# Kernel tuning notes

Measured on AMD Instinct MI355X. Metric: run time of the kernel, lower is better.

## Reference

```python
import jax, jax.numpy as jnp
import numpy as np

NT = ['SB', 'PQ', 'PV', 'NB']
SIZES = {'SB': 4000, 'PQ': 30000, 'PV': 15000, 'NB': 12000}
ETYPES = [('PV','SB'),('SB','PQ'),('SB','NB'),('PV','PQ'),('NB','PQ'),('PQ','NB'),('SB','PV'),('PQ','SB'),('NB','SB'),('PQ','PV'),('PV','NB'),('NB','PV'),('PV','PV'),('PQ','PQ'),('NB','NB')]
L, H, O, F, E, ED = 2, 128, 64, 8, 150000, 2
T = len(ETYPES)


def setup_inputs():
    key = jax.random.key(0)
    ks = iter(jax.random.split(key, 80))
    inp = {}
    for nt in NT:
        inp['x_' + nt] = jax.random.normal(next(ks), (SIZES[nt], 4), jnp.float32)
        inp['c_' + nt] = jax.random.normal(next(ks), (SIZES[nt], 4), jnp.float32)
    ei = []
    for (s, d) in ETYPES:
        ei.append(jnp.stack([jax.random.randint(next(ks), (E,), 0, SIZES[s]),
                             jax.random.randint(next(ks), (E,), 0, SIZES[d])]))
    inp['edge_index'] = jnp.stack(ei).astype(jnp.int32)  # [T, 2, E]
    inp['edge_attr'] = jax.random.normal(next(ks), (T, E, ED), jnp.float32)
    p = lambda k, *s: jax.random.normal(k, s, jnp.float32) * 0.1
    inp['Wq'] = p(next(ks), L, T, F, H); inp['bq'] = jnp.zeros((L, T, H), jnp.float32)
    inp['Wk'] = p(next(ks), L, T, F, H); inp['bk'] = jnp.zeros((L, T, H), jnp.float32)
    inp['Wv'] = p(next(ks), L, T, F, H); inp['bv'] = jnp.zeros((L, T, H), jnp.float32)
    inp['We'] = p(next(ks), L, T, ED, H); inp['be'] = jnp.zeros((L, T, H), jnp.float32)
    inp['Ws'] = p(next(ks), L, T, F, H); inp['bs'] = jnp.zeros((L, T, H), jnp.float32)
    inp['W_lin'] = p(next(ks), 2, O); inp['b_lin'] = jnp.zeros((O,), jnp.float32)
    inp['W_fc'] = p(next(ks), len(NT), O, O); inp['b_fc'] = jnp.zeros((len(NT), O), jnp.float32)
    inp['W_lin2'] = p(next(ks), 2, O); inp['b_lin2'] = jnp.zeros((O,), jnp.float32)
    return inp


def _tconv(xs, xd, src, dst, ea, Wq, bq, Wk, bk, Wv, bv, We, be, Ws, bs):
    # PyG TransformerConv, heads=1, edge_dim=2, root_weight=True, beta=False
    nd = xd.shape[0]
    q = xd @ Wq + bq            # [Nd, H]
    k = xs @ Wk + bk            # [Ns, H]
    v = xs @ Wv + bv            # [Ns, H]
    e = ea @ We + be            # [E, H]
    kj = k[src] + e
    vj = v[src] + e
    logit = (q[dst] * kj).sum(-1) / np.float32(np.sqrt(q.shape[-1]))  # [E]
    m = jax.ops.segment_max(logit, dst, num_segments=nd)
    pe = jnp.exp(logit - m[dst])
    den = jax.ops.segment_sum(pe, dst, num_segments=nd)
    alpha = pe / (den[dst] + 1e-16)  # PyG softmax epsilon
    agg = jax.ops.segment_sum(alpha[:, None] * vj, dst, num_segments=nd)
    return agg + xd @ Ws + bs   # skip connection (lin_skip)


def _group_sum(xs):
    # 'group': cat on node axis, split channels in half (P/Q), sum each half
    out = jnp.concatenate(xs, axis=0)
    half = out.shape[1] // 2
    return jnp.stack([out[:, :half].sum(1), out[:, half:].sum(1)], axis=1)  # [M, 2]


def reference(x_SB, x_PQ, x_PV, x_NB, c_SB, c_PQ, c_PV, c_NB, edge_index, edge_attr,
              Wq, bq, Wk, bk, Wv, bv, We, be, Ws, bs,
              W_lin, b_lin, W_fc, b_fc, W_lin2, b_lin2):
    xmap = {'SB': (x_SB, c_SB), 'PQ': (x_PQ, c_PQ), 'PV': (x_PV, c_PV), 'NB': (x_NB, c_NB)}
    x = {nt: jnp.concatenate(xmap[nt], axis=1) for nt in NT}  # [N, 8]
    outs = {nt: [] for nt in NT}
    for i in range(L):
        for t, (s, d) in enumerate(ETYPES):
            outs[d].append(_tconv(x[s], x[d], edge_index[t, 0], edge_index[t, 1], edge_attr[t],
                                  Wq[i, t], bq[i, t], Wk[i, t], bk[i, t], Wv[i, t], bv[i, t],
                                  We[i, t], be[i, t], Ws[i, t], bs[i, t]))
    agg = {nt: jax.nn.elu(_group_sum(outs[nt]) @ W_lin + b_lin) for nt in NT}
    # HeteroMinMaxNorm with running_min=0, running_max=1, momentum=0.1 (updated then used)
    xc = jnp.concatenate([agg[nt] for nt in NT], axis=0)
    rmin = 0.1 * xc.min()
    rmax = 0.9 + 0.1 * xc.max()
    xsc = (xc - rmin) / (rmax - rmin + 1e-5) * 2.0 - 1.0
    sizes = [agg[nt].shape[0] for nt in NT]
    splits = jnp.split(xsc, np.cumsum(sizes)[:-1].tolist(), axis=0)
    nrm = dict(zip(NT, splits))
    node_lists = {nt: [] for nt in NT}
    for i in range(L):
        for j, nt in enumerate(NT):
            node_lists[nt].append(jax.nn.elu(nrm[nt] @ W_fc[j] + b_fc[j]))
    final = [jax.nn.elu(_group_sum(node_lists[nt]) @ W_lin2 + b_lin2) for nt in NT]
    return jnp.concatenate(final, axis=0)  # [960000, 64]
```

## Files before the change

### kernel.cpp

```cpp
#include <hip/hip_runtime.h>
#include <hip/hip_fp16.h>
#include <math.h>

#define NE 150000

__constant__ int c_stype[15] = {2,0,0,2,3,1,0,1,3,1,2,3,2,1,3};
__constant__ int c_dtype[15] = {0,1,3,1,1,3,2,0,0,2,3,2,2,1,3};
__constant__ int c_slot[15]  = {0,0,0,1,2,1,0,1,2,1,2,2,3,3,3};
__constant__ int c_N[4]      = {4000,30000,15000,12000};
__constant__ int c_xoff[4]   = {0,4000,34000,49000};
__constant__ int c_cnt[4]    = {3,4,4,4};
__constant__ int c_aggoff[4] = {0,24000,264000,384000};
__constant__ int c_outoff[4] = {0,48000,528000,768000};
__constant__ int c_aggrows[4]= {24000,240000,120000,96000};
__constant__ int c_lT[4] = {7,10,9,9};
__constant__ int c_tprefix[16] = {0,32,62,86,116,146,170,200,232,264,294,318,348,378,408,432};
__constant__ int c_toff2[15] = {0,4001,34002,46003,76004,106005,118006,133007,137008,141009,156010,168011,183012,198013,228014};

typedef _Float16 f16x8 __attribute__((ext_vector_type(8)));
typedef float f32x4 __attribute__((ext_vector_type(4)));

__device__ __forceinline__ float eluf(float x){ return x > 0.0f ? x : expm1f(x); }
__device__ __forceinline__ float elufast(float x){ return x > 0.0f ? x : __expf(x)-1.0f; }
__device__ __forceinline__ unsigned encf(float f){ unsigned u=__float_as_uint(f); return (u&0x80000000u)? ~u : (u|0x80000000u); }
__device__ __forceinline__ float decf(unsigned u){ return __uint_as_float((u&0x80000000u)? (u^0x80000000u) : ~u); }
__device__ __forceinline__ float RL(float v, int l){ return __uint_as_float(__builtin_amdgcn_readlane(__float_as_uint(v), l)); }

__device__ __forceinline__ float dot128(const float* __restrict__ a, const float* __restrict__ b){
  const float4* a4 = (const float4*)a; const float4* b4 = (const float4*)b;
  float s = 0.f;
  #pragma unroll
  for (int h=0; h<32; h++){
    float4 A=a4[h], B=b4[h];
    s = fmaf(A.x,B.x,s); s = fmaf(A.y,B.y,s); s = fmaf(A.z,B.z,s); s = fmaf(A.w,B.w,s);
  }
  return s;
}
__device__ __forceinline__ void halfsum(const float* __restrict__ a, float& s0, float& s1){
  const float4* a4 = (const float4*)a;
  float x0=0.f, x1=0.f;
  #pragma unroll
  for (int h=0; h<16; h++){ float4 A=a4[h]; x0 += A.x+A.y+A.z+A.w; }
  #pragma unroll
  for (int h=16; h<32; h++){ float4 A=a4[h]; x1 += A.x+A.y+A.z+A.w; }
  s0=x0; s1=x1;
}

#define CHUNK 18750

__global__ __launch_bounds__(1024) void k_front(
    const float* __restrict__ xSB, const float* __restrict__ cSB,
    const float* __restrict__ xPQ, const float* __restrict__ cPQ,
    const float* __restrict__ xPV, const float* __restrict__ cPV,
    const float* __restrict__ xNB, const float* __restrict__ cNB,
    const int* __restrict__ eidx,
    const float* __restrict__ Wq, const float* __restrict__ bq,
    const float* __restrict__ Wk, const float* __restrict__ bk,
    const float* __restrict__ Wv, const float* __restrict__ bv,
    const float* __restrict__ We, const float* __restrict__ be,
    const float* __restrict__ Ws, const float* __restrict__ bs,
    float* __restrict__ xall, float* __restrict__ par, int* __restrict__ gcnt8){
  const int b = blockIdx.x;
  if (b < 60){
    const int n = b*1024 + threadIdx.x;
    if (n >= 61000) return;
    const float *xp, *cp; int local;
    if (n < 4000)      { xp=xSB; cp=cSB; local=n; }
    else if (n < 34000){ xp=xPQ; cp=cPQ; local=n-4000; }
    else if (n < 49000){ xp=xPV; cp=cPV; local=n-34000; }
    else               { xp=xNB; cp=cNB; local=n-49000; }
    float4 a = ((const float4*)xp)[local];
    float4 bb = ((const float4*)cp)[local];
    ((float4*)xall)[n*2+0] = a;
    ((float4*)xall)[n*2+1] = bb;
  } else if (b < 90){
    const int c = b - 60, tid = threadIdx.x;
    if (tid >= 128) return;
    const float* wq = Wq + (size_t)c*1024;
    const float* wk = Wk + (size_t)c*1024;
    const float* wv = Wv + (size_t)c*1024;
    const float* ws = Ws + (size_t)c*1024;
    const float* we = We + (size_t)c*256;
    const float* vbq = bq + (size_t)c*128;
    const float* vbk = bk + (size_t)c*128;
    const float* vbv = bv + (size_t)c*128;
    const float* vbe = be + (size_t)c*128;
    const float* vbs = bs + (size_t)c*128;
    float* P = par + (size_t)c*160;
    if (tid < 64){
      int fd = tid>>3, fs = tid&7;
      P[tid] = dot128(wq + fd*128, wk + fs*128);
      return;
    }
    const int job = tid - 64, grp = job>>3, f = job&7;
    if (grp==0) P[64+f] = dot128(wq + f*128, vbk);
    else if (grp==1) P[72+f] = dot128(wk + f*128, vbq);
    else if (grp==2) P[80+f] = dot128(wq + f*128, we);
    else if (grp==3) P[88+f] = dot128(wq + f*128, we+128);
    else if (grp==4) P[96+f] = dot128(wq + f*128, vbe);
    else if (grp==5){ float s0,s1; halfsum(wv + f*128, s0,s1); P[104+f]=s0; P[112+f]=s1; }
    else if (grp==6){ float s0,s1; halfsum(ws + f*128, s0,s1); P[120+f]=s0; P[128+f]=s1; }
    else {
      if (f==0){ P[136] = dot128(vbq, vbk);
                 float a,bb; halfsum(vbs, a,bb); P[148]=a; P[149]=bb; }
      else if (f==1) P[137] = dot128(vbq, we);
      else if (f==2) P[138] = dot128(vbq, we+128);
      else if (f==3) P[139] = dot128(vbq, vbe);
      else if (f==4){ float a=0.f,bb=0.f; for(int h=0;h<64;h++){a+=we[h]; bb+=we[64+h];} P[140]=a; P[141]=bb; }
      else if (f==5){ float a=0.f,bb=0.f; for(int h=0;h<64;h++){a+=we[128+h]; bb+=we[192+h];} P[142]=a; P[143]=bb; }
      else if (f==6){ float a,bb; halfsum(vbv, a,bb); P[144]=a; P[145]=bb; }
      else          { float a,bb; halfsum(vbe, a,bb); P[146]=a; P[147]=bb; }
    }
  } else {
    const int cb = b - 90;
    const int t = cb / 8, chunk = cb % 8;
    const int lT = c_lT[c_dtype[t]];
    __shared__ int scnt[32];
    if (threadIdx.x < 32) scnt[threadIdx.x] = 0;
    __syncthreads();
    const int* __restrict__ dstp = eidx + (size_t)(t*2+1)*NE;
    const int e0 = chunk*CHUNK, e1 = min(NE, e0+CHUNK);
    for (int e=e0+threadIdx.x; e<e1; e+=1024) atomicAdd(&scnt[dstp[e]>>lT], 1);
    __syncthreads();
    if (threadIdx.x < 32) gcnt8[(t*8 + chunk)*32 + threadIdx.x] = scnt[threadIdx.x];
  }
}

__global__ void k_scan(const int* __restrict__ gcnt8, int* __restrict__ gcnt,
                       int* __restrict__ gofs, int* __restrict__ gcur,
                       unsigned* __restrict__ mm){
  const int t = threadIdx.x;
  if (t == 16){ mm[0] = 0xFFFFFFFFu; }
  else if (t == 17){ mm[1] = 0u; }
  if (t >= 15) return;
  const int b0 = c_tprefix[t], b1 = c_tprefix[t+1];
  int run = t*NE;
  for (int b=b0; b<b1; b++){
    const int tile = b - b0;
    int c0 = 0;
    #pragma unroll
    for (int c=0; c<8; c++) c0 += gcnt8[(t*8 + c)*32 + tile];
    gcnt[b] = c0;
    gofs[b] = run; gcur[b] = run;
    run += c0;
  }
}

__global__ __launch_bounds__(1024) void k_scatter(const int* __restrict__ eidx,
    const float* __restrict__ eattr,
    int* __restrict__ gcur, uint2* __restrict__ ebuf){
  const int t = blockIdx.y;
  const int lT = c_lT[c_dtype[t]];
  const int tmask = (1<<lT) - 1;
  __shared__ int lcnt[32], lbase[32];
  if (threadIdx.x < 32) lcnt[threadIdx.x] = 0;
  __syncthreads();
  const int* __restrict__ dstp = eidx + (size_t)(t*2+1)*NE;
  const int* __restrict__ srcp = eidx + (size_t)(t*2)*NE;
  const float2* __restrict__ ea2 = (const float2*)eattr + (size_t)t*NE;
  const int e0 = blockIdx.x*CHUNK, e1 = min(NE, e0+CHUNK);
  for (int e=e0+threadIdx.x; e<e1; e+=1024) atomicAdd(&lcnt[dstp[e]>>lT], 1);
  __syncthreads();
  if (threadIdx.x < 32){
    int cchk = lcnt[threadIdx.x];
    lbase[threadIdx.x] = cchk > 0 ? atomicAdd(&gcur[c_tprefix[t]+threadIdx.x], cchk) : 0;
  }
  __syncthreads();
  if (threadIdx.x < 32) lcnt[threadIdx.x] = 0;
  __syncthreads();
  for (int e=e0+threadIdx.x; e<e1; e+=1024){
    const int d = dstp[e];
    const int tile = d>>lT, dl = d & tmask;
    const int pos = lbase[tile] + atomicAdd(&lcnt[tile], 1);
    const float2 ea = ea2[e];
    __half2 h2 = __floats2half2_rn(ea.x, ea.y);
    ebuf[pos] = make_uint2(((unsigned)srcp[e]<<10) | (unsigned)dl, *(unsigned*)&h2);
  }
}

__global__ __launch_bounds__(1024) void k_tsort(
    const uint2* __restrict__ ebuf,
    const int* __restrict__ gofs, const int* __restrict__ gcnt,
    uint2* __restrict__ erec, int* __restrict__ gs2, int* __restrict__ glen){
  const int b = blockIdx.x;
  int t = 0;
  while (b >= c_tprefix[t+1]) ++t;
  const int tile = b - c_tprefix[t];
  const int dt = c_dtype[t];
  const int N = c_N[dt];
  const int lT = c_lT[dt];
  const int nbase = tile << lT;
  const int tileN = min(1<<lT, N - nbase);
  const int tid = threadIdx.x;
  const int lane = tid & 63, wid = tid >> 6;

  __shared__ int cnt[1024];
  __shared__ int wsum[16];

  cnt[tid] = 0;
  __syncthreads();
  const int start = gofs[b], count = gcnt[b];
  for (int k=tid; k<count; k+=1024) atomicAdd(&cnt[ebuf[start+k].x & 1023u], 1);
  __syncthreads();
  const int v = cnt[tid];
  int inc = v;
  #pragma unroll
  for (int off=1; off<64; off<<=1){ int u = __shfl_up(inc, off); if (lane>=off) inc += u; }
  if (lane==63) wsum[wid] = inc;
  __syncthreads();
  if (tid==0){ int r=0; for (int k=0;k<16;k++){ int x=wsum[k]; wsum[k]=r; r+=x; } }
  __syncthreads();
  const int pref = wsum[wid] + inc - v;
  if (tid < tileN){
    gs2 [c_toff2[t] + nbase + tid] = start + pref;
    glen[c_toff2[t] + nbase + tid] = v;
  }
  cnt[tid] = pref;
  __syncthreads();
  for (int k=tid; k<count; k+=1024){
    const uint2 u2 = ebuf[start+k];
    const int dl = u2.x & 1023u;
    const int pos = start + atomicAdd(&cnt[dl], 1);
    erec[pos] = make_uint2(u2.x >> 10, u2.y);
  }
}

__global__ __launch_bounds__(256) void k_gather(
    const int* __restrict__ gs2, const int* __restrict__ glen,
    const uint2* __restrict__ erec,
    const float* __restrict__ xall, const float* __restrict__ par,
    const float* __restrict__ Wl, const float* __restrict__ bl,
    float* __restrict__ g, unsigned* __restrict__ mm){
  const int t = blockIdx.y;
  const int dt = c_dtype[t], st = c_stype[t];
  const int N = c_N[dt];
  if (blockIdx.x*256 >= N) return;
  __shared__ float sA[160], sB[160];
  __shared__ float wlb[192];
  __shared__ float smin[4], smax[4];
  const int tid = threadIdx.x;
  if (tid < 160){ sA[tid] = par[(size_t)t*160 + tid]; sB[tid] = par[(size_t)(15+t)*160 + tid]; }
  if (tid < 192) wlb[tid] = (tid<128)? Wl[tid] : bl[tid-128];
  __syncthreads();
  const int n = blockIdx.x*256 + tid;
  const bool valid = n < N;
  float lmin = 3.4e38f, lmax = -3.4e38f;
  if (valid){
    const float4* xdp = (const float4*)(xall + (size_t)(c_xoff[dt]+n)*8);
    float4 b0v = xdp[0], b1v = xdp[1];
    float xd[8] = {b0v.x,b0v.y,b0v.z,b0v.w,b1v.x,b1v.y,b1v.z,b1v.w};
    float r2a[8], r2b[8];
    #pragma unroll
    for (int fs=0; fs<8; fs++){
      float a = sA[72+fs], bb = sB[72+fs];
      #pragma unroll
      for (int fd=0; fd<8; fd++){ a = fmaf(xd[fd], sA[fd*8+fs], a); bb = fmaf(xd[fd], sB[fd*8+fs], bb); }
      r2a[fs]=a; r2b[fs]=bb;
    }
    float t0a=sA[137], t1a=sA[138], tba=sA[139], u0a=sA[136];
    float t0b=sB[137], t1b=sB[138], tbb=sB[139], u0b=sB[136];
    #pragma unroll
    for (int f=0;f<8;f++){
      t0a = fmaf(xd[f], sA[80+f], t0a);  t0b = fmaf(xd[f], sB[80+f], t0b);
      t1a = fmaf(xd[f], sA[88+f], t1a);  t1b = fmaf(xd[f], sB[88+f], t1b);
      tba = fmaf(xd[f], sA[96+f], tba);  tbb = fmaf(xd[f], sB[96+f], tbb);
      u0a = fmaf(xd[f], sA[64+f], u0a);  u0b = fmaf(xd[f], sB[64+f], u0b);
    }
    const float accda = u0a + tba, accdb = u0b + tbb;
    const int o = c_toff2[t];
    const int js = gs2[o+n], je = js + glen[o+n];
    float denA=0.f, n0A=0.f, n1A=0.f;
    float denB=0.f, n0B=0.f, n1B=0.f;
    if (je > js){
      uint2 rec = erec[js];
      const float4* xp0 = (const float4*)(xall + (size_t)(c_xoff[st]+(int)rec.x)*8);
      float4 xa = xp0[0], xb = xp0[1];
      for (int j=js; j<je; j++){
        const int jn = (j+1 < je) ? j+1 : j;
        const uint2 recn = erec[jn];
        const float4* xpn = (const float4*)(xall + (size_t)(c_xoff[st]+(int)recn.x)*8);
        const float4 xan = xpn[0], xbn = xpn[1];
        const __half2 h2 = *(const __half2*)&rec.y;
        const float eax = __low2float(h2), eay = __high2float(h2);
        float xs[8] = {xa.x,xa.y,xa.z,xa.w,xb.x,xb.y,xb.z,xb.w};
        float accA = accda, accB = accdb;
        float v0A = fmaf(eax, sA[140], fmaf(eay, sA[142], sA[144]+sA[146]));
        float v1A = fmaf(eax, sA[141], fmaf(eay, sA[143], sA[145]+sA[147]));
        float v0B = fmaf(eax, sB[140], fmaf(eay, sB[142], sB[144]+sB[146]));
        float v1B = fmaf(eax, sB[141], fmaf(eay, sB[143], sB[145]+sB[147]));
        #pragma unroll
        for (int f=0;f<8;f++){
          accA = fmaf(xs[f], r2a[f], accA);   accB = fmaf(xs[f], r2b[f], accB);
          v0A  = fmaf(xs[f], sA[104+f], v0A); v0B  = fmaf(xs[f], sB[104+f], v0B);
          v1A  = fmaf(xs[f], sA[112+f], v1A); v1B  = fmaf(xs[f], sB[112+f], v1B);
        }
        accA = fmaf(eax, t0a, fmaf(eay, t1a, accA));
        accB = fmaf(eax, t0b, fmaf(eay, t1b, accB));
        const float peA = __expf(accA * 0.08838834764831845f);
        const float peB = __expf(accB * 0.08838834764831845f);
        denA += peA; n0A = fmaf(peA, v0A, n0A); n1A = fmaf(peA, v1A, n1A);
        denB += peB; n0B = fmaf(peB, v0B, n0B); n1B = fmaf(peB, v1B, n1B);
        rec = recn; xa = xan; xb = xbn;
      }
    }
    const float invA = 1.0f/(denA + 1e-16f);
    const float invB = 1.0f/(denB + 1e-16f);
    float s0a = fmaf(n0A, invA, sA[148]), s1a = fmaf(n1A, invA, sA[149]);
    float s0b = fmaf(n0B, invB, sB[148]), s1b = fmaf(n1B, invB, sB[149]);
    #pragma unroll
    for (int f=0;f<8;f++){
      s0a = fmaf(xd[f], sA[120+f], s0a); s1a = fmaf(xd[f], sA[128+f], s1a);
      s0b = fmaf(xd[f], sB[120+f], s0b); s1b = fmaf(xd[f], sB[128+f], s1b);
    }
    const int baseA = c_aggoff[dt] + (0*c_cnt[dt] + c_slot[t])*N + n;
    const int baseB = c_aggoff[dt] + (1*c_cnt[dt] + c_slot[t])*N + n;
    ((float2*)g)[baseA] = make_float2(s0a, s1a);
    ((float2*)g)[baseB] = make_float2(s0b, s1b);
    #pragma unroll
    for (int h=0;h<64;h++){
      float za = fmaf(s0a, wlb[h], fmaf(s1a, wlb[64+h], wlb[128+h]));
      float zb = fmaf(s0b, wlb[h], fmaf(s1b, wlb[64+h], wlb[128+h]));
      lmin = fminf(lmin, fminf(za,zb)); lmax = fmaxf(lmax, fmaxf(za,zb));
    }
  }
  #pragma unroll
  for (int m=32;m>=1;m>>=1){
    lmin = fminf(lmin, __shfl_xor(lmin,m));
    lmax = fmaxf(lmax, __shfl_xor(lmax,m));
  }
  const int wv = tid>>6;
  if ((tid&63)==0){ smin[wv]=lmin; smax[wv]=lmax; }
  __syncthreads();
  if (tid==0){
    float mn = fminf(fminf(smin[0],smin[1]), fminf(smin[2],smin[3]));
    float mx = fmaxf(fmaxf(smax[0],smax[1]), fmaxf(smax[2],smax[3]));
    atomicMin(&mm[0], encf(mn));
    atomicMax(&mm[1], encf(mx));
  }
}

__global__ __launch_bounds__(256) void k_final(
    const float* __restrict__ g, const unsigned* __restrict__ mm,
    const float* __restrict__ Wl, const float* __restrict__ bl,
    const float* __restrict__ Wfc, const float* __restrict__ bfc,
    const float* __restrict__ Wl2, const float* __restrict__ bl2,
    float* __restrict__ out){
  const int gw = blockIdx.x*4 + (threadIdx.x>>6);
  const int l  = threadIdx.x & 63;
  const int lr = l & 15, lg = l >> 4;
  int nt, wo;
  if (gw < 375)       { nt=0; wo=0; }
  else if (gw < 4125) { nt=1; wo=375; }
  else if (gw < 6000) { nt=2; wo=4125; }
  else                { nt=3; wo=6000; }
  const int R = c_aggrows[nt];
  const int r0 = (gw - wo)*64;
  const float zmin = decf(mm[0]), zmax = decf(mm[1]);
  const float rmin = 0.1f*eluf(zmin);
  const float rmax = 0.9f + 0.1f*eluf(zmax);
  const float s2 = 2.0f/(rmax - rmin + 1e-5f);
  const float cc = fmaf(-rmin, s2, -1.0f);
  float wl0v[2][8], wl1v[2][8], blv[2][8];
  #pragma unroll
  for (int kk=0; kk<2; kk++){
    const int hb = kk*32 + lg*8;
    const float4 a0 = *(const float4*)&Wl[hb],    a1 = *(const float4*)&Wl[hb+4];
    const float4 b0 = *(const float4*)&Wl[64+hb], b1 = *(const float4*)&Wl[64+hb+4];
    const float4 c0 = *(const float4*)&bl[hb],    c1 = *(const float4*)&bl[hb+4];
    wl0v[kk][0]=a0.x; wl0v[kk][1]=a0.y; wl0v[kk][2]=a0.z; wl0v[kk][3]=a0.w;
    wl0v[kk][4]=a1.x; wl0v[kk][5]=a1.y; wl0v[kk][6]=a1.z; wl0v[kk][7]=a1.w;
    wl1v[kk][0]=b0.x; wl1v[kk][1]=b0.y; wl1v[kk][2]=b0.z; wl1v[kk][3]=b0.w;
    wl1v[kk][4]=b1.x; wl1v[kk][5]=b1.y; wl1v[kk][6]=b1.z; wl1v[kk][7]=b1.w;
    blv[kk][0]=c0.x;  blv[kk][1]=c0.y;  blv[kk][2]=c0.z;  blv[kk][3]=c0.w;
    blv[kk][4]=c1.x;  blv[kk][5]=c1.y;  blv[kk][6]=c1.z;  blv[kk][7]=c1.w;
  }
  const float* __restrict__ W = Wfc + (size_t)nt*4096;
  f16x8 bfrag[2][4];
  #pragma unroll
  for (int kk=0; kk<2; kk++){
    #pragma unroll
    for (int ntl=0; ntl<4; ntl++){
      #pragma unroll
      for (int j=0; j<8; j++){
        const int h = kk*32 + lg*8 + j;
        bfrag[kk][ntl][j] = (_Float16)W[h*64 + ntl*16 + lr];
      }
    }
  }
  const float bf0 = bfc[nt*64 + lr],      bf1 = bfc[nt*64 + 16 + lr];
  const float bf2 = bfc[nt*64 + 32 + lr], bf3 = bfc[nt*64 + 48 + lr];
  const float2* __restrict__ g2p = (const float2*)g + c_aggoff[nt] + r0;
  const float wl20 = Wl2[l], wl21 = Wl2[64+l], bl2v = bl2[l];
  float* __restrict__ o1 = out + ((size_t)c_outoff[nt] + r0)*64 + l;
  float* __restrict__ o2 = o1 + (size_t)R*64;
  #pragma unroll
  for (int mt=0; mt<4; mt++){
    const float2 gv = g2p[mt*16 + lr];
    f16x8 af0, af1;
    #pragma unroll
    for (int j=0; j<8; j++){
      const float z0 = fmaf(gv.x, wl0v[0][j], fmaf(gv.y, wl1v[0][j], blv[0][j]));
      const float z1 = fmaf(gv.x, wl0v[1][j], fmaf(gv.y, wl1v[1][j], blv[1][j]));
      af0[j] = (_Float16)fmaf(elufast(z0), s2, cc);
      af1[j] = (_Float16)fmaf(elufast(z1), s2, cc);
    }
    f32x4 d0 = {0.f,0.f,0.f,0.f}, d1 = {0.f,0.f,0.f,0.f};
    f32x4 d2 = {0.f,0.f,0.f,0.f}, d3 = {0.f,0.f,0.f,0.f};
    d0 = __builtin_amdgcn_mfma_f32_16x16x32_f16(af0, bfrag[0][0], d0, 0,0,0);
    d1 = __builtin_amdgcn_mfma_f32_16x16x32_f16(af0, bfrag[0][1], d1, 0,0,0);
    d2 = __builtin_amdgcn_mfma_f32_16x16x32_f16(af0, bfrag[0][2], d2, 0,0,0);
    d3 = __builtin_amdgcn_mfma_f32_16x16x32_f16(af0, bfrag[0][3], d3, 0,0,0);
    d0 = __builtin_amdgcn_mfma_f32_16x16x32_f16(af1, bfrag[1][0], d0, 0,0,0);
    d1 = __builtin_amdgcn_mfma_f32_16x16x32_f16(af1, bfrag[1][1], d1, 0,0,0);
    d2 = __builtin_amdgcn_mfma_f32_16x16x32_f16(af1, bfrag[1][2], d2, 0,0,0);
    d3 = __builtin_amdgcn_mfma_f32_16x16x32_f16(af1, bfrag[1][3], d3, 0,0,0);
    float ph0[4], ph1[4];
    #pragma unroll
    for (int reg=0; reg<4; reg++){
      float p0 = elufast(d0[reg] + bf0) + elufast(d1[reg] + bf1);
      float p1 = elufast(d2[reg] + bf2) + elufast(d3[reg] + bf3);
      p0 += __shfl_xor(p0,1); p0 += __shfl_xor(p0,2); p0 += __shfl_xor(p0,4); p0 += __shfl_xor(p0,8);
      p1 += __shfl_xor(p1,1); p1 += __shfl_xor(p1,2); p1 += __shfl_xor(p1,4); p1 += __shfl_xor(p1,8);
      ph0[reg] = p0; ph1[reg] = p1;
    }
    #pragma unroll
    for (int rt=0; rt<16; rt++){
      const int r = mt*16 + rt;
      const float h0r = RL(ph0[rt&3], (rt>>2)<<4);
      const float h1r = RL(ph1[rt&3], (rt>>2)<<4);
      const float f = elufast(fmaf(h0r, wl20, fmaf(h1r, wl21, bl2v)));
      o1[(size_t)r*64] = f;
      o2[(size_t)r*64] = f;
    }
  }
}

extern "C" void kernel_launch(void* const* d_in, const int* in_sizes, int n_in,
                              void* d_out, int out_size, void* d_ws, size_t ws_size,
                              hipStream_t stream) {
  const float* xSB = (const float*)d_in[0];
  const float* cSB = (const float*)d_in[1];
  const float* xPQ = (const float*)d_in[2];
  const float* cPQ = (const float*)d_in[3];
  const float* xPV = (const float*)d_in[4];
  const float* cPV = (const float*)d_in[5];
  const float* xNB = (const float*)d_in[6];
  const float* cNB = (const float*)d_in[7];
  const int*   eidx = (const int*)d_in[8];
  const float* eattr= (const float*)d_in[9];
  const float* Wq = (const float*)d_in[10];
  const float* bq = (const float*)d_in[11];
  const float* Wk = (const float*)d_in[12];
  const float* bk = (const float*)d_in[13];
  const float* Wv = (const float*)d_in[14];
  const float* bv = (const float*)d_in[15];
  const float* We = (const float*)d_in[16];
  const float* be = (const float*)d_in[17];
  const float* Ws = (const float*)d_in[18];
  const float* bs = (const float*)d_in[19];
  const float* Wl = (const float*)d_in[20];
  const float* bl = (const float*)d_in[21];
  const float* Wfc= (const float*)d_in[22];
  const float* bfc= (const float*)d_in[23];
  const float* Wl2= (const float*)d_in[24];
  const float* bl2= (const float*)d_in[25];

  float* ws    = (float*)d_ws;
  float* xall  = ws + 0;
  float* par   = ws + 488000;
  int* gs2     = (int*)(ws + 492800);
  int* glen    = (int*)(ws + 732815);
  int* gcnt    = (int*)(ws + 972830);
  int* gofs    = (int*)(ws + 973262);
  int* gcur    = (int*)(ws + 973694);
  unsigned* mm = (unsigned*)(ws + 974126);
  int* gcnt8   = (int*)(ws + 974128);
  uint2* ebuf  = (uint2*)(ws + 977968);
  uint2* erec  = (uint2*)(ws + 5477968);
  float* g     = ws + 9977968;

  k_front<<<210, 1024, 0, stream>>>(xSB,cSB,xPQ,cPQ,xPV,cPV,xNB,cNB, eidx,
                                    Wq,bq,Wk,bk,Wv,bv,We,be,Ws,bs,
                                    xall, par, gcnt8);
  k_scan<<<1, 64, 0, stream>>>(gcnt8, gcnt, gofs, gcur, mm);
  dim3 gb(8, 15);
  k_scatter<<<gb, 1024, 0, stream>>>(eidx, eattr, gcur, ebuf);
  k_tsort<<<432, 1024, 0, stream>>>(ebuf, gofs, gcnt, erec, gs2, glen);
  dim3 gg(118, 15);
  k_gather<<<gg, 256, 0, stream>>>(gs2, glen, erec, xall, par, Wl, bl, g, mm);
  k_final<<<1875, 256, 0, stream>>>(g, mm, Wl, bl, Wfc, bfc, Wl2, bl2, (float*)d_out);
}
```

Before: 207.4 us.

## Unroll edge gather loop by four with prefetch; vectorize final output stores

The per-destination edge loop now processes four edges per iteration and prefetches the next four edge records and source features, with masking for the tail. The goal is more memory-level parallelism on the irregular gathers. The final kernel stages the per-row reduced values in shared memory, so each lane writes float4 chunks instead of scalar strided stores. This cuts store instruction count and improves coalescing, at the cost of more registers in the edge loop and wasted compute on padded tail edges.

```diff
diff --git a/kernel.cpp b/kernel.cpp
--- a/kernel.cpp
+++ b/kernel.cpp
@@ -269,40 +269,66 @@
     const float accda = u0a + tba, accdb = u0b + tbb;
     const int o = c_toff2[t];
     const int js = gs2[o+n], je = js + glen[o+n];
+    const int xo = c_xoff[st];
     float denA=0.f, n0A=0.f, n1A=0.f;
     float denB=0.f, n0B=0.f, n1B=0.f;
+
+#define GCOMP(RV, XA, XB, JJ)                                              \
+    {                                                                      \
+      const float mk = ((JJ) < je) ? 1.0f : 0.0f;                          \
+      const __half2 h2c = *(const __half2*)&RV.y;                          \
+      const float eax = __low2float(h2c), eay = __high2float(h2c);         \
+      float xs[8] = {XA.x,XA.y,XA.z,XA.w,XB.x,XB.y,XB.z,XB.w};             \
+      float accA = accda, accB = accdb;                                    \
+      float v0A = fmaf(eax, sA[140], fmaf(eay, sA[142], sA[144]+sA[146])); \
+      float v1A = fmaf(eax, sA[141], fmaf(eay, sA[143], sA[145]+sA[147])); \
+      float v0B = fmaf(eax, sB[140], fmaf(eay, sB[142], sB[144]+sB[146])); \
+      float v1B = fmaf(eax, sB[141], fmaf(eay, sB[143], sB[145]+sB[147])); \
+      _Pragma("unroll")                                                    \
+      for (int f=0;f<8;f++){                                               \
+        accA = fmaf(xs[f], r2a[f], accA);   accB = fmaf(xs[f], r2b[f], accB); \
+        v0A  = fmaf(xs[f], sA[104+f], v0A); v0B  = fmaf(xs[f], sB[104+f], v0B); \
+        v1A  = fmaf(xs[f], sA[112+f], v1A); v1B  = fmaf(xs[f], sB[112+f], v1B); \
+      }                                                                    \
+      accA = fmaf(eax, t0a, fmaf(eay, t1a, accA));                         \
+      accB = fmaf(eax, t0b, fmaf(eay, t1b, accB));                         \
+      const float peA = __expf(accA * 0.08838834764831845f) * mk;          \
+      const float peB = __expf(accB * 0.08838834764831845f) * mk;          \
+      denA += peA; n0A = fmaf(peA, v0A, n0A); n1A = fmaf(peA, v1A, n1A);   \
+      denB += peB; n0B = fmaf(peB, v0B, n0B); n1B = fmaf(peB, v1B, n1B);   \
+    }
+
     if (je > js){
-      uint2 rec = erec[js];
-      const float4* xp0 = (const float4*)(xall + (size_t)(c_xoff[st]+(int)rec.x)*8);
-      float4 xa = xp0[0], xb = xp0[1];
-      for (int j=js; j<je; j++){
-        const int jn = (j+1 < je) ? j+1 : j;
-        const uint2 recn = erec[jn];
-        const float4* xpn = (const float4*)(xall + (size_t)(c_xoff[st]+(int)recn.x)*8);
-        const float4 xan = xpn[0], xbn = xpn[1];
-        const __half2 h2 = *(const __half2*)&rec.y;
-        const float eax = __low2float(h2), eay = __high2float(h2);
-        float xs[8] = {xa.x,xa.y,xa.z,xa.w,xb.x,xb.y,xb.z,xb.w};
-        float accA = accda, accB = accdb;
-        float v0A = fmaf(eax, sA[140], fmaf(eay, sA[142], sA[144]+sA[146]));
-        float v1A = fmaf(eax, sA[141], fmaf(eay, sA[143], sA[145]+sA[147]));
-        float v0B = fmaf(eax, sB[140], fmaf(eay, sB[142], sB[144]+sB[146]));
-        float v1B = fmaf(eax, sB[141], fmaf(eay, sB[143], sB[145]+sB[147]));
-        #pragma unroll
-        for (int f=0;f<8;f++){
-          accA = fmaf(xs[f], r2a[f], accA);   accB = fmaf(xs[f], r2b[f], accB);
-          v0A  = fmaf(xs[f], sA[104+f], v0A); v0B  = fmaf(xs[f], sB[104+f], v0B);
-          v1A  = fmaf(xs[f], sA[112+f], v1A); v1B  = fmaf(xs[f], sB[112+f], v1B);
-        }
-        accA = fmaf(eax, t0a, fmaf(eay, t1a, accA));
-        accB = fmaf(eax, t0b, fmaf(eay, t1b, accB));
-        const float peA = __expf(accA * 0.08838834764831845f);
-        const float peB = __expf(accB * 0.08838834764831845f);
-        denA += peA; n0A = fmaf(peA, v0A, n0A); n1A = fmaf(peA, v1A, n1A);
-        denB += peB; n0B = fmaf(peB, v0B, n0B); n1B = fmaf(peB, v1B, n1B);
-        rec = recn; xa = xan; xb = xbn;
+      const int jl = je - 1;
+      uint2 r0 = erec[js];
+      uint2 r1 = erec[min(js+1, jl)];
+      uint2 r2 = erec[min(js+2, jl)];
+      uint2 r3 = erec[min(js+3, jl)];
+      const float4* p;
+      p = (const float4*)(xall + (size_t)(xo+(int)r0.x)*8); float4 xa0=p[0], xb0=p[1];
+      p = (const float4*)(xall + (size_t)(xo+(int)r1.x)*8); float4 xa1=p[0], xb1=p[1];
+      p = (const float4*)(xall + (size_t)(xo+(int)r2.x)*8); float4 xa2=p[0], xb2=p[1];
+      p = (const float4*)(xall + (size_t)(xo+(int)r3.x)*8); float4 xa3=p[0], xb3=p[1];
+      for (int j0=js; j0<je; j0+=4){
+        const int jn = j0 + 4;
+        const uint2 n0r = erec[min(jn,   jl)];
+        const uint2 n1r = erec[min(jn+1, jl)];
+        const uint2 n2r = erec[min(jn+2, jl)];
+        const uint2 n3r = erec[min(jn+3, jl)];
+        GCOMP(r0, xa0, xb0, j0+0)
+        p = (const float4*)(xall + (size_t)(xo+(int)n0r.x)*8); const float4 ya0=p[0], yb0=p[1];
+        p = (const float4*)(xall + (size_t)(xo+(int)n1r.x)*8); const float4 ya1=p[0], yb1=p[1];
+        p = (const float4*)(xall + (size_t)(xo+(int)n2r.x)*8); const float4 ya2=p[0], yb2=p[1];
+        p = (const float4*)(xall + (size_t)(xo+(int)n3r.x)*8); const float4 ya3=p[0], yb3=p[1];
+        GCOMP(r1, xa1, xb1, j0+1)
+        GCOMP(r2, xa2, xb2, j0+2)
+        GCOMP(r3, xa3, xb3, j0+3)
+        r0=n0r; r1=n1r; r2=n2r; r3=n3r;
+        xa0=ya0; xb0=yb0; xa1=ya1; xb1=yb1;
+        xa2=ya2; xb2=yb2; xa3=ya3; xb3=yb3;
       }
     }
+#undef GCOMP
     const float invA = 1.0f/(denA + 1e-16f);
     const float invB = 1.0f/(denB + 1e-16f);
     float s0a = fmaf(n0A, invA, sA[148]), s1a = fmaf(n1A, invA, sA[149]);
@@ -348,6 +374,8 @@
   const int gw = blockIdx.x*4 + (threadIdx.x>>6);
   const int l  = threadIdx.x & 63;
   const int lr = l & 15, lg = l >> 4;
+  const int wv = threadIdx.x >> 6;
+  __shared__ float lh0[4][64], lh1[4][64];
   int nt, wo;
   if (gw < 375)       { nt=0; wo=0; }
   else if (gw < 4125) { nt=1; wo=375; }
@@ -390,9 +418,6 @@
   const float bf0 = bfc[nt*64 + lr],      bf1 = bfc[nt*64 + 16 + lr];
   const float bf2 = bfc[nt*64 + 32 + lr], bf3 = bfc[nt*64 + 48 + lr];
   const float2* __restrict__ g2p = (const float2*)g + c_aggoff[nt] + r0;
-  const float wl20 = Wl2[l], wl21 = Wl2[64+l], bl2v = bl2[l];
-  float* __restrict__ o1 = out + ((size_t)c_outoff[nt] + r0)*64 + l;
-  float* __restrict__ o2 = o1 + (size_t)R*64;
   #pragma unroll
   for (int mt=0; mt<4; mt++){
     const float2 gv = g2p[mt*16 + lr];
@@ -423,15 +448,31 @@
       p1 += __shfl_xor(p1,1); p1 += __shfl_xor(p1,2); p1 += __shfl_xor(p1,4); p1 += __shfl_xor(p1,8);
       ph0[reg] = p0; ph1[reg] = p1;
     }
-    #pragma unroll
-    for (int rt=0; rt<16; rt++){
-      const int r = mt*16 + rt;
-      const float h0r = RL(ph0[rt&3], (rt>>2)<<4);
-      const float h1r = RL(ph1[rt&3], (rt>>2)<<4);
-      const float f = elufast(fmaf(h0r, wl20, fmaf(h1r, wl21, bl2v)));
-      o1[(size_t)r*64] = f;
-      o2[(size_t)r*64] = f;
-    }
+    if (lr == 0){
+      const int rb = mt*16 + lg*4;
+      lh0[wv][rb+0]=ph0[0]; lh0[wv][rb+1]=ph0[1]; lh0[wv][rb+2]=ph0[2]; lh0[wv][rb+3]=ph0[3];
+      lh1[wv][rb+0]=ph1[0]; lh1[wv][rb+1]=ph1[1]; lh1[wv][rb+2]=ph1[2]; lh1[wv][rb+3]=ph1[3];
+    }
+  }
+  const int rs = l >> 4;
+  const int quad = l & 15;
+  const float4 w2a = *(const float4*)&Wl2[quad*4];
+  const float4 w2b = *(const float4*)&Wl2[64 + quad*4];
+  const float4 b2v = *(const float4*)&bl2[quad*4];
+  float* __restrict__ obase = out + ((size_t)c_outoff[nt] + r0)*64;
+  #pragma unroll
+  for (int it=0; it<16; it++){
+    const int r = it*4 + rs;
+    const float h0 = lh0[wv][r], h1 = lh1[wv][r];
+    float4 fo;
+    fo.x = elufast(fmaf(h0, w2a.x, fmaf(h1, w2b.x, b2v.x)));
+    fo.y = elufast(fmaf(h0, w2a.y, fmaf(h1, w2b.y, b2v.y)));
+    fo.z = elufast(fmaf(h0, w2a.z, fmaf(h1, w2b.z, b2v.z)));
+    fo.w = elufast(fmaf(h0, w2a.w, fmaf(h1, w2b.w, b2v.w)));
+    float4* p1 = (float4*)(obase + (size_t)r*64 + quad*4);
+    float4* p2 = (float4*)((float*)p1 + (size_t)R*64);
+    *p1 = fo;
+    *p2 = fo;
   }
 }
 
```

New measurement: 214.1 us. +3.2%, slower.

## Compute edge logits in scatter and reduce per-tile with shared atomics

Applied to the files above, without the earlier changes.

Edge logits, exponentials and value projections for both layers are now computed in the scatter kernel and written as packed per-edge records. A new per-tile reduce kernel accumulates softmax denominators and numerators with shared-memory float atomics. This replaces the per-destination counting sort and the gather kernel, removing one pass over the edges and the random source loads inside per-node serial loops. In exchange, each edge record grows to 20 bytes, and the reduce relies on heavily contended LDS atomics. The softmax also runs without max subtraction, as it did before.

```diff
diff --git a/kernel.cpp b/kernel.cpp
--- a/kernel.cpp
+++ b/kernel.cpp
@@ -15,7 +15,6 @@
 __constant__ int c_aggrows[4]= {24000,240000,120000,96000};
 __constant__ int c_lT[4] = {7,10,9,9};
 __constant__ int c_tprefix[16] = {0,32,62,86,116,146,170,200,232,264,294,318,348,378,408,432};
-__constant__ int c_toff2[15] = {0,4001,34002,46003,76004,106005,118006,133007,137008,141009,156010,168011,183012,198013,228014};
 
 typedef _Float16 f16x8 __attribute__((ext_vector_type(8)));
 typedef float f32x4 __attribute__((ext_vector_type(4)));
@@ -147,13 +146,18 @@
 }
 
 __global__ __launch_bounds__(1024) void k_scatter(const int* __restrict__ eidx,
-    const float* __restrict__ eattr,
-    int* __restrict__ gcur, uint2* __restrict__ ebuf){
+    const float* __restrict__ eattr, const float* __restrict__ xall,
+    const float* __restrict__ par,
+    int* __restrict__ gcur, uint4* __restrict__ ebufA, unsigned* __restrict__ ebufD){
   const int t = blockIdx.y;
-  const int lT = c_lT[c_dtype[t]];
+  const int dt = c_dtype[t], st = c_stype[t];
+  const int lT = c_lT[dt];
   const int tmask = (1<<lT) - 1;
   __shared__ int lcnt[32], lbase[32];
+  __shared__ float sA[160], sB[160];
   if (threadIdx.x < 32) lcnt[threadIdx.x] = 0;
+  if (threadIdx.x >= 64 && threadIdx.x < 224) sA[threadIdx.x-64] = par[(size_t)t*160 + threadIdx.x-64];
+  if (threadIdx.x >= 224 && threadIdx.x < 384) sB[threadIdx.x-224] = par[(size_t)(15+t)*160 + threadIdx.x-224];
   __syncthreads();
   const int* __restrict__ dstp = eidx + (size_t)(t*2+1)*NE;
   const int* __restrict__ srcp = eidx + (size_t)(t*2)*NE;
@@ -168,20 +172,68 @@
   __syncthreads();
   if (threadIdx.x < 32) lcnt[threadIdx.x] = 0;
   __syncthreads();
+  const int xod = c_xoff[dt], xos = c_xoff[st];
+  const float SCALE = 0.08838834764831845f;
   for (int e=e0+threadIdx.x; e<e1; e+=1024){
     const int d = dstp[e];
     const int tile = d>>lT, dl = d & tmask;
     const int pos = lbase[tile] + atomicAdd(&lcnt[tile], 1);
     const float2 ea = ea2[e];
-    __half2 h2 = __floats2half2_rn(ea.x, ea.y);
-    ebuf[pos] = make_uint2(((unsigned)srcp[e]<<10) | (unsigned)dl, *(unsigned*)&h2);
-  }
-}
-
-__global__ __launch_bounds__(1024) void k_tsort(
-    const uint2* __restrict__ ebuf,
+    const float4* xdp = (const float4*)(xall + (size_t)(xod+d)*8);
+    const float4* xsp = (const float4*)(xall + (size_t)(xos+srcp[e])*8);
+    const float4 d0v = xdp[0], d1v = xdp[1];
+    const float4 s0v = xsp[0], s1v = xsp[1];
+    float xd[8] = {d0v.x,d0v.y,d0v.z,d0v.w,d1v.x,d1v.y,d1v.z,d1v.w};
+    float xs[8] = {s0v.x,s0v.y,s0v.z,s0v.w,s1v.x,s1v.y,s1v.z,s1v.w};
+    float accA = sA[136], t0a = sA[137], t1a = sA[138], tba = sA[139];
+    float accB = sB[136], t0b = sB[137], t1b = sB[138], tbb = sB[139];
+    #pragma unroll
+    for (int fd=0; fd<8; fd++){
+      float ta = 0.f, tb2 = 0.f;
+      #pragma unroll
+      for (int fs=0; fs<8; fs++){ ta = fmaf(sA[fd*8+fs], xs[fs], ta); tb2 = fmaf(sB[fd*8+fs], xs[fs], tb2); }
+      accA = fmaf(xd[fd], ta, accA);
+      accB = fmaf(xd[fd], tb2, accB);
+    }
+    float v0A = fmaf(ea.x, sA[140], fmaf(ea.y, sA[142], sA[144]+sA[146]));
+    float v1A = fmaf(ea.x, sA[141], fmaf(ea.y, sA[143], sA[145]+sA[147]));
+    float v0B = fmaf(ea.x, sB[140], fmaf(ea.y, sB[142], sB[144]+sB[146]));
+    float v1B = fmaf(ea.x, sB[141], fmaf(ea.y, sB[143], sB[145]+sB[147]));
+    #pragma unroll
+    for (int f=0; f<8; f++){
+      accA = fmaf(xd[f], sA[64+f], accA);
+      accA = fmaf(xs[f], sA[72+f], accA);
+      t0a  = fmaf(xd[f], sA[80+f], t0a);
+      t1a  = fmaf(xd[f], sA[88+f], t1a);
+      tba  = fmaf(xd[f], sA[96+f], tba);
+      v0A  = fmaf(xs[f], sA[104+f], v0A);
+      v1A  = fmaf(xs[f], sA[112+f], v1A);
+      accB = fmaf(xd[f], sB[64+f], accB);
+      accB = fmaf(xs[f], sB[72+f], accB);
+      t0b  = fmaf(xd[f], sB[80+f], t0b);
+      t1b  = fmaf(xd[f], sB[88+f], t1b);
+      tbb  = fmaf(xd[f], sB[96+f], tbb);
+      v0B  = fmaf(xs[f], sB[104+f], v0B);
+      v1B  = fmaf(xs[f], sB[112+f], v1B);
+    }
+    accA += fmaf(ea.x, t0a, fmaf(ea.y, t1a, tba));
+    accB += fmaf(ea.x, t0b, fmaf(ea.y, t1b, tbb));
+    const float peA = __expf(accA * SCALE);
+    const float peB = __expf(accB * SCALE);
+    __half2 hA = __floats2half2_rn(v0A, v1A);
+    __half2 hB = __floats2half2_rn(v0B, v1B);
+    ebufA[pos] = make_uint4(__float_as_uint(peA), __float_as_uint(peB),
+                            *(unsigned*)&hA, *(unsigned*)&hB);
+    ebufD[pos] = (unsigned)dl;
+  }
+}
+
+__global__ __launch_bounds__(1024) void k_reduce(
+    const uint4* __restrict__ ebufA, const unsigned* __restrict__ ebufD,
     const int* __restrict__ gofs, const int* __restrict__ gcnt,
-    uint2* __restrict__ erec, int* __restrict__ gs2, int* __restrict__ glen){
+    const float* __restrict__ xall, const float* __restrict__ par,
+    const float* __restrict__ Wl, const float* __restrict__ bl,
+    float* __restrict__ g, unsigned* __restrict__ mm){
   const int b = blockIdx.x;
   int t = 0;
   while (b >= c_tprefix[t+1]) ++t;
@@ -192,117 +244,44 @@
   const int nbase = tile << lT;
   const int tileN = min(1<<lT, N - nbase);
   const int tid = threadIdx.x;
-  const int lane = tid & 63, wid = tid >> 6;
-
-  __shared__ int cnt[1024];
-  __shared__ int wsum[16];
-
-  cnt[tid] = 0;
-  __syncthreads();
+
+  __shared__ float ACC[6144];
+  __shared__ float sA[160], sB[160], wlb[192];
+  __shared__ float smin[16], smax[16];
+
+  for (int k=tid; k<6144; k+=1024) ACC[k] = 0.f;
+  if (tid >= 64 && tid < 224) sA[tid-64] = par[(size_t)t*160 + tid-64];
+  if (tid >= 224 && tid < 384) sB[tid-224] = par[(size_t)(15+t)*160 + tid-224];
+  if (tid >= 384 && tid < 576){ int u=tid-384; wlb[u] = (u<128)? Wl[u] : bl[u-128]; }
+  __syncthreads();
+
   const int start = gofs[b], count = gcnt[b];
-  for (int k=tid; k<count; k+=1024) atomicAdd(&cnt[ebuf[start+k].x & 1023u], 1);
-  __syncthreads();
-  const int v = cnt[tid];
-  int inc = v;
-  #pragma unroll
-  for (int off=1; off<64; off<<=1){ int u = __shfl_up(inc, off); if (lane>=off) inc += u; }
-  if (lane==63) wsum[wid] = inc;
-  __syncthreads();
-  if (tid==0){ int r=0; for (int k=0;k<16;k++){ int x=wsum[k]; wsum[k]=r; r+=x; } }
-  __syncthreads();
-  const int pref = wsum[wid] + inc - v;
+  for (int k=tid; k<count; k+=1024){
+    const unsigned dl = ebufD[start+k];
+    const uint4 u4 = ebufA[start+k];
+    const float peA = __uint_as_float(u4.x);
+    const float peB = __uint_as_float(u4.y);
+    const float2 vA = __half22float2(*(const __half2*)&u4.z);
+    const float2 vB = __half22float2(*(const __half2*)&u4.w);
+    float* a = &ACC[dl*6];
+    atomicAdd(a+0, peA);
+    atomicAdd(a+1, peA*vA.x);
+    atomicAdd(a+2, peA*vA.y);
+    atomicAdd(a+3, peB);
+    atomicAdd(a+4, peB*vB.x);
+    atomicAdd(a+5, peB*vB.y);
+  }
+  __syncthreads();
+
+  float lmin = 3.4e38f, lmax = -3.4e38f;
   if (tid < tileN){
-    gs2 [c_toff2[t] + nbase + tid] = start + pref;
-    glen[c_toff2[t] + nbase + tid] = v;
-  }
-  cnt[tid] = pref;
-  __syncthreads();
-  for (int k=tid; k<count; k+=1024){
-    const uint2 u2 = ebuf[start+k];
-    const int dl = u2.x & 1023u;
-    const int pos = start + atomicAdd(&cnt[dl], 1);
-    erec[pos] = make_uint2(u2.x >> 10, u2.y);
-  }
-}
-
-__global__ __launch_bounds__(256) void k_gather(
-    const int* __restrict__ gs2, const int* __restrict__ glen,
-    const uint2* __restrict__ erec,
-    const float* __restrict__ xall, const float* __restrict__ par,
-    const float* __restrict__ Wl, const float* __restrict__ bl,
-    float* __restrict__ g, unsigned* __restrict__ mm){
-  const int t = blockIdx.y;
-  const int dt = c_dtype[t], st = c_stype[t];
-  const int N = c_N[dt];
-  if (blockIdx.x*256 >= N) return;
-  __shared__ float sA[160], sB[160];
-  __shared__ float wlb[192];
-  __shared__ float smin[4], smax[4];
-  const int tid = threadIdx.x;
-  if (tid < 160){ sA[tid] = par[(size_t)t*160 + tid]; sB[tid] = par[(size_t)(15+t)*160 + tid]; }
-  if (tid < 192) wlb[tid] = (tid<128)? Wl[tid] : bl[tid-128];
-  __syncthreads();
-  const int n = blockIdx.x*256 + tid;
-  const bool valid = n < N;
-  float lmin = 3.4e38f, lmax = -3.4e38f;
-  if (valid){
+    const int n = nbase + tid;
     const float4* xdp = (const float4*)(xall + (size_t)(c_xoff[dt]+n)*8);
-    float4 b0v = xdp[0], b1v = xdp[1];
+    const float4 b0v = xdp[0], b1v = xdp[1];
     float xd[8] = {b0v.x,b0v.y,b0v.z,b0v.w,b1v.x,b1v.y,b1v.z,b1v.w};
-    float r2a[8], r2b[8];
-    #pragma unroll
-    for (int fs=0; fs<8; fs++){
-      float a = sA[72+fs], bb = sB[72+fs];
-      #pragma unroll
-      for (int fd=0; fd<8; fd++){ a = fmaf(xd[fd], sA[fd*8+fs], a); bb = fmaf(xd[fd], sB[fd*8+fs], bb); }
-      r2a[fs]=a; r2b[fs]=bb;
-    }
-    float t0a=sA[137], t1a=sA[138], tba=sA[139], u0a=sA[136];
-    float t0b=sB[137], t1b=sB[138], tbb=sB[139], u0b=sB[136];
-    #pragma unroll
-    for (int f=0;f<8;f++){
-      t0a = fmaf(xd[f], sA[80+f], t0a);  t0b = fmaf(xd[f], sB[80+f], t0b);
-      t1a = fmaf(xd[f], sA[88+f], t1a);  t1b = fmaf(xd[f], sB[88+f], t1b);
-      tba = fmaf(xd[f], sA[96+f], tba);  tbb = fmaf(xd[f], sB[96+f], tbb);
-      u0a = fmaf(xd[f], sA[64+f], u0a);  u0b = fmaf(xd[f], sB[64+f], u0b);
-    }
-    const float accda = u0a + tba, accdb = u0b + tbb;
-    const int o = c_toff2[t];
-    const int js = gs2[o+n], je = js + glen[o+n];
-    float denA=0.f, n0A=0.f, n1A=0.f;
-    float denB=0.f, n0B=0.f, n1B=0.f;
-    if (je > js){
-      uint2 rec = erec[js];
-      const float4* xp0 = (const float4*)(xall + (size_t)(c_xoff[st]+(int)rec.x)*8);
-      float4 xa = xp0[0], xb = xp0[1];
-      for (int j=js; j<je; j++){
-        const int jn = (j+1 < je) ? j+1 : j;
-        const uint2 recn = erec[jn];
-        const float4* xpn = (const float4*)(xall + (size_t)(c_xoff[st]+(int)recn.x)*8);
-        const float4 xan = xpn[0], xbn = xpn[1];
-        const __half2 h2 = *(const __half2*)&rec.y;
-        const float eax = __low2float(h2), eay = __high2float(h2);
-        float xs[8] = {xa.x,xa.y,xa.z,xa.w,xb.x,xb.y,xb.z,xb.w};
-        float accA = accda, accB = accdb;
-        float v0A = fmaf(eax, sA[140], fmaf(eay, sA[142], sA[144]+sA[146]));
-        float v1A = fmaf(eax, sA[141], fmaf(eay, sA[143], sA[145]+sA[147]));
-        float v0B = fmaf(eax, sB[140], fmaf(eay, sB[142], sB[144]+sB[146]));
-        float v1B = fmaf(eax, sB[141], fmaf(eay, sB[143], sB[145]+sB[147]));
-        #pragma unroll
-        for (int f=0;f<8;f++){
-          accA = fmaf(xs[f], r2a[f], accA);   accB = fmaf(xs[f], r2b[f], accB);
-          v0A  = fmaf(xs[f], sA[104+f], v0A); v0B  = fmaf(xs[f], sB[104+f], v0B);
-          v1A  = fmaf(xs[f], sA[112+f], v1A); v1B  = fmaf(xs[f], sB[112+f], v1B);
-        }
-        accA = fmaf(eax, t0a, fmaf(eay, t1a, accA));
-        accB = fmaf(eax, t0b, fmaf(eay, t1b, accB));
-        const float peA = __expf(accA * 0.08838834764831845f);
-        const float peB = __expf(accB * 0.08838834764831845f);
-        denA += peA; n0A = fmaf(peA, v0A, n0A); n1A = fmaf(peA, v1A, n1A);
-        denB += peB; n0B = fmaf(peB, v0B, n0B); n1B = fmaf(peB, v1B, n1B);
-        rec = recn; xa = xan; xb = xbn;
-      }
-    }
+    const float* a = &ACC[tid*6];
+    const float denA = a[0], n0A = a[1], n1A = a[2];
+    const float denB = a[3], n0B = a[4], n1B = a[5];
     const float invA = 1.0f/(denA + 1e-16f);
     const float invB = 1.0f/(denB + 1e-16f);
     float s0a = fmaf(n0A, invA, sA[148]), s1a = fmaf(n1A, invA, sA[149]);
@@ -332,8 +311,8 @@
   if ((tid&63)==0){ smin[wv]=lmin; smax[wv]=lmax; }
   __syncthreads();
   if (tid==0){
-    float mn = fminf(fminf(smin[0],smin[1]), fminf(smin[2],smin[3]));
-    float mx = fmaxf(fmaxf(smax[0],smax[1]), fmaxf(smax[2],smax[3]));
+    float mn = smin[0], mx = smax[0];
+    for (int k=1;k<16;k++){ mn = fminf(mn, smin[k]); mx = fmaxf(mx, smax[k]); }
     atomicMin(&mm[0], encf(mn));
     atomicMax(&mm[1], encf(mx));
   }
@@ -468,25 +447,21 @@
   float* ws    = (float*)d_ws;
   float* xall  = ws + 0;
   float* par   = ws + 488000;
-  int* gs2     = (int*)(ws + 492800);
-  int* glen    = (int*)(ws + 732815);
-  int* gcnt    = (int*)(ws + 972830);
-  int* gofs    = (int*)(ws + 973262);
-  int* gcur    = (int*)(ws + 973694);
-  unsigned* mm = (unsigned*)(ws + 974126);
-  int* gcnt8   = (int*)(ws + 974128);
-  uint2* ebuf  = (uint2*)(ws + 977968);
-  uint2* erec  = (uint2*)(ws + 5477968);
-  float* g     = ws + 9977968;
+  int* gcnt    = (int*)(ws + 492800);
+  int* gofs    = (int*)(ws + 493232);
+  int* gcur    = (int*)(ws + 493664);
+  unsigned* mm = (unsigned*)(ws + 494096);
+  int* gcnt8   = (int*)(ws + 494100);
+  uint4* ebufA = (uint4*)(ws + 497944);
+  unsigned* ebufD = (unsigned*)(ws + 9497944);
+  float* g     = ws + 11747944;
 
   k_front<<<210, 1024, 0, stream>>>(xSB,cSB,xPQ,cPQ,xPV,cPV,xNB,cNB, eidx,
                                     Wq,bq,Wk,bk,Wv,bv,We,be,Ws,bs,
                                     xall, par, gcnt8);
   k_scan<<<1, 64, 0, stream>>>(gcnt8, gcnt, gofs, gcur, mm);
   dim3 gb(8, 15);
-  k_scatter<<<gb, 1024, 0, stream>>>(eidx, eattr, gcur, ebuf);
-  k_tsort<<<432, 1024, 0, stream>>>(ebuf, gofs, gcnt, erec, gs2, glen);
-  dim3 gg(118, 15);
-  k_gather<<<gg, 256, 0, stream>>>(gs2, glen, erec, xall, par, Wl, bl, g, mm);
+  k_scatter<<<gb, 1024, 0, stream>>>(eidx, eattr, xall, par, gcur, ebufA, ebufD);
+  k_reduce<<<432, 1024, 0, stream>>>(ebufA, ebufD, gofs, gcnt, xall, par, Wl, bl, g, mm);
   k_final<<<1875, 256, 0, stream>>>(g, mm, Wl, bl, Wfc, bfc, Wl2, bl2, (float*)d_out);
 }
```

Result: slower. 642.1 us (+209.5%).
